# Optimization experiments

Measured on AMD Instinct MI355X. Metric: run time of the kernel, lower is better.

The kernel has to match this reference:

```python
import jax, jax.numpy as jnp
import numpy as np

H = 512; NH = 8; L = 2; NPRED = 26; MAXF = 5; FF = 4 * H


def _ln(x, w, b, eps=1e-5):
    m = x.mean(-1, keepdims=True)
    v = ((x - m) ** 2).mean(-1, keepdims=True)
    return (x - m) / jnp.sqrt(v + eps) * w + b


def _gelu(x):
    return jax.nn.gelu(x, approximate=False)


def _mha(q_in, kv_in, in_w, in_b, out_w, out_b, nh=NH):
    # PyTorch nn.MultiheadAttention math (batch_first), no mask, eval mode.
    h = q_in.shape[-1]; dh = h // nh
    Wq, Wk, Wv = in_w[:h], in_w[h:2 * h], in_w[2 * h:]
    bq, bk, bv = in_b[:h], in_b[h:2 * h], in_b[2 * h:]
    B, Tq, _ = q_in.shape
    Tk = kv_in.shape[1]
    q = (q_in @ Wq.T + bq).reshape(B, Tq, nh, dh)
    k = (kv_in @ Wk.T + bk).reshape(B, Tk, nh, dh)
    v = (kv_in @ Wv.T + bv).reshape(B, Tk, nh, dh)
    s = jnp.einsum('bqhd,bkhd->bhqk', q, k) / jnp.sqrt(jnp.asarray(dh, q.dtype))
    a = jax.nn.softmax(s, axis=-1)
    o = jnp.einsum('bhqk,bkhd->bqhd', a, v).reshape(B, Tq, h)
    return o @ out_w.T + out_b


def setup_inputs():
    key = jax.random.key(0)
    ks = iter(jax.random.split(key, 48))
    r = lambda *s: jax.random.normal(next(ks), s, jnp.float32) * 0.02
    inp = {
        'temporal_context': jax.random.normal(next(ks), (16, 10, H), jnp.float32),
        'object_features': jax.random.normal(next(ks), (16, 20, H), jnp.float32),
        'future_queries': r(MAXF, H),
        'sa_in_w': r(L, 3 * H, H), 'sa_in_b': jnp.zeros((L, 3 * H), jnp.float32),
        'sa_out_w': r(L, H, H), 'sa_out_b': jnp.zeros((L, H), jnp.float32),
        'ca_in_w': r(L, 3 * H, H), 'ca_in_b': jnp.zeros((L, 3 * H), jnp.float32),
        'ca_out_w': r(L, H, H), 'ca_out_b': jnp.zeros((L, H), jnp.float32),
        'ff1_w': r(L, FF, H), 'ff1_b': jnp.zeros((L, FF), jnp.float32),
        'ff2_w': r(L, H, FF), 'ff2_b': jnp.zeros((L, H), jnp.float32),
        'n1_w': jnp.ones((L, H), jnp.float32), 'n1_b': jnp.zeros((L, H), jnp.float32),
        'n2_w': jnp.ones((L, H), jnp.float32), 'n2_b': jnp.zeros((L, H), jnp.float32),
        'n3_w': jnp.ones((L, H), jnp.float32), 'n3_b': jnp.zeros((L, H), jnp.float32),
        'norm_w': jnp.ones((H,), jnp.float32), 'norm_b': jnp.zeros((H,), jnp.float32),
        'pe1_w': r(H, 3 * H), 'pe1_b': jnp.zeros((H,), jnp.float32),
        'pe2_w': r(H, H), 'pe2_b': jnp.zeros((H,), jnp.float32),
        'pred_w': r(NPRED, H), 'pred_b': jnp.zeros((NPRED,), jnp.float32),
        'ex_w': r(1, H), 'ex_b': jnp.zeros((1,), jnp.float32),
        'num_future_frames': 5,
    }
    return inp


def reference(temporal_context, object_features, future_queries, sa_in_w, sa_in_b,
              sa_out_w, sa_out_b, ca_in_w, ca_in_b, ca_out_w, ca_out_b,
              ff1_w, ff1_b, ff2_w, ff2_b, n1_w, n1_b, n2_w, n2_b, n3_w, n3_b,
              norm_w, norm_b, pe1_w, pe1_b, pe2_w, pe2_b, pred_w, pred_b,
              ex_w, ex_b, num_future_frames):
    B = temporal_context.shape[0]
    Fh = num_future_frames
    # Future queries expanded over batch -> TransformerDecoder (post-norm, gelu, eval)
    x = jnp.broadcast_to(future_queries[:Fh][None], (B, Fh, H))
    mem = temporal_context
    for l in range(L):
        x = _ln(x + _mha(x, x, sa_in_w[l], sa_in_b[l], sa_out_w[l], sa_out_b[l]), n1_w[l], n1_b[l])
        x = _ln(x + _mha(x, mem, ca_in_w[l], ca_in_b[l], ca_out_w[l], ca_out_b[l]), n2_w[l], n2_b[l])
        ff = _gelu(x @ ff1_w[l].T + ff1_b[l]) @ ff2_w[l].T + ff2_b[l]
        x = _ln(x + ff, n3_w[l], n3_b[l])
    ctx = _ln(x, norm_w, norm_b)  # (B, F, H)
    # Vectorized (i, j) pair construction, i != j, in the original loop order
    N = object_features.shape[1]
    ii, jj = np.nonzero(~np.eye(N, dtype=bool))  # row-major == for i: for j: skip i==j
    P = ii.shape[0]
    subj = object_features[:, ii]  # (B, P, H)
    obj = object_features[:, jj]   # (B, P, H)
    pair = jnp.concatenate([
        jnp.broadcast_to(subj[:, None], (B, Fh, P, H)),
        jnp.broadcast_to(obj[:, None], (B, Fh, P, H)),
        jnp.broadcast_to(ctx[:, :, None], (B, Fh, P, H)),
    ], axis=-1)  # (B, F, P, 3H)
    enc = _gelu(pair @ pe1_w.T + pe1_b) @ pe2_w.T + pe2_b  # (B, F, P, H)
    predicate_logits = enc @ pred_w.T + pred_b  # (B, F, P, 26)
    existence_logits = enc @ ex_w.T + ex_b      # (B, F, P, 1)
    return predicate_logits, existence_logits
```

## Files before the change

kernel.cpp:

```cpp
#include <hip/hip_runtime.h>
#include <math.h>

#define HD 512
#define FFD 2048
#define FH 5
#define TM 10
#define NO 20
#define NP 380
#define PRED_N 790400

#define XM_PLAIN 0
#define XM_GELU  1
#define XM_FQ    2
#define XM_LN    3
#define XM_LN2   4

typedef short bf16x8 __attribute__((ext_vector_type(8)));
typedef float floatx4 __attribute__((ext_vector_type(4)));

__device__ __forceinline__ float gelu_f(float v) {
    return 0.5f * v * (1.0f + erff(v * 0.70710678118654752440f));
}
__device__ __forceinline__ unsigned short f2bf(float x) {
    unsigned int u = __float_as_uint(x);
    u = (u + 0x7FFFu + ((u >> 16) & 1u)) >> 16;
    return (unsigned short)u;
}

template <int XMODE>
__device__ __forceinline__ void gemm_body(
    int bx, int by, int bz,
    const float* __restrict__ X, int ldx,
    const float* __restrict__ parts, int np, int pzstr,
    const float* __restrict__ bo,
    const float* __restrict__ lw, const float* __restrict__ lb,
    const float* __restrict__ fw, const float* __restrict__ fb,
    float* __restrict__ xout, int xmod, int gps,
    const float* __restrict__ W, int ldw,
    float* __restrict__ Y, int ldy, int zyoff,
    int Klen, float* lds)
{
    float* Wt = lds;
    float* Xs = lds + 8256;
    const int RT = (XMODE >= XM_LN) ? 8 : 16;
    int t = threadIdx.x;
    int nb = bx * 128;
    int r0 = by * RT;
    int kbase = bz * Klen;
    float* Yb = Y + (size_t)bz * zyoff;
    int c = t & 31, rg = t >> 5, scs = t >> 4, q = t & 15;

    if (XMODE >= XM_LN) {
        int rl = t >> 5;
        int r  = r0 + rl;
        int c0 = (t & 31) * 16;
        int rr = xmod ? (r % xmod) : r;
        float v[16];
        #pragma unroll
        for (int u = 0; u < 16; u += 4) {
            float4 a = *(const float4*)(X + (size_t)rr * ldx + c0 + u);
            float4 bb = *(const float4*)(bo + c0 + u);
            float vx = a.x + bb.x, vy = a.y + bb.y, vz = a.z + bb.z, vw = a.w + bb.w;
            for (int zz = 0; zz < np; ++zz) {
                float4 p = *(const float4*)(parts + (size_t)zz * pzstr + (size_t)r * HD + c0 + u);
                vx += p.x; vy += p.y; vz += p.z; vw += p.w;
            }
            v[u] = vx; v[u + 1] = vy; v[u + 2] = vz; v[u + 3] = vw;
        }
        float s1 = 0, s2 = 0;
        #pragma unroll
        for (int u = 0; u < 16; ++u) { s1 += v[u]; s2 += v[u] * v[u]; }
        #pragma unroll
        for (int o = 16; o > 0; o >>= 1) {
            s1 += __shfl_down(s1, o, 32);
            s2 += __shfl_down(s2, o, 32);
        }
        s1 = __shfl(s1, 0, 32); s2 = __shfl(s2, 0, 32);
        float mean = s1 * (1.0f / HD);
        float rstd = rsqrtf(s2 * (1.0f / HD) - mean * mean + 1e-5f);
        #pragma unroll
        for (int u = 0; u < 16; ++u)
            v[u] = (v[u] - mean) * rstd * lw[c0 + u] + lb[c0 + u];
        if (xout && bz == 0 && bx == 0) {
            #pragma unroll
            for (int u = 0; u < 16; u += 4)
                *(float4*)(xout + (size_t)r * HD + c0 + u) =
                    make_float4(v[u], v[u + 1], v[u + 2], v[u + 3]);
        }
        if (XMODE == XM_LN2) {
            float t1 = 0, t2 = 0;
            #pragma unroll
            for (int u = 0; u < 16; ++u) { t1 += v[u]; t2 += v[u] * v[u]; }
            #pragma unroll
            for (int o = 16; o > 0; o >>= 1) {
                t1 += __shfl_down(t1, o, 32);
                t2 += __shfl_down(t2, o, 32);
            }
            t1 = __shfl(t1, 0, 32); t2 = __shfl(t2, 0, 32);
            float m2 = t1 * (1.0f / HD);
            float rs2 = rsqrtf(t2 * (1.0f / HD) - m2 * m2 + 1e-5f);
            #pragma unroll
            for (int u = 0; u < 16; ++u)
                v[u] = (v[u] - m2) * rs2 * fw[c0 + u] + fb[c0 + u];
        }
        #pragma unroll
        for (int u = 0; u < 16; u += 4)
            *(float4*)(Xs + rl * HD + c0 + u) =
                make_float4(v[u], v[u + 1], v[u + 2], v[u + 3]);
        __syncthreads();
    }

    float a00 = 0, a01 = 0, a02 = 0, a03 = 0;
    float a10 = 0, a11 = 0, a12 = 0, a13 = 0;

    int nch = Klen >> 6;
    float4 wreg[8];
    float4 xra, xrb, xrc;
    {
        int kg = kbase;
        #pragma unroll
        for (int p = 0; p < 8; ++p)
            wreg[p] = *(const float4*)(W + (size_t)(nb + scs + p * 16) * ldw + kg + q * 4);
        if (XMODE == XM_PLAIN) {
            xra = *(const float4*)(X + (size_t)(r0 + scs) * ldx + kg + q * 4);
        } else if (XMODE == XM_FQ) {
            xra = *(const float4*)(X + (size_t)((r0 + scs) % FH) * ldx + kg + q * 4);
        } else if (XMODE == XM_GELU) {
            const float* p0 = X + (size_t)(r0 + scs) * ldx + kg + q * 4;
            xra = *(const float4*)p0;
            xrb = *(const float4*)(p0 + gps);
            xrc = *(const float4*)(bo + kg + q * 4);
        }
    }

    for (int ch = 0; ch < nch; ++ch) {
        if (ch) __syncthreads();
        if (XMODE <= XM_FQ) {
            float4 xv;
            if (XMODE == XM_GELU) {
                xv.x = gelu_f(xra.x + xrb.x + xrc.x);
                xv.y = gelu_f(xra.y + xrb.y + xrc.y);
                xv.z = gelu_f(xra.z + xrb.z + xrc.z);
                xv.w = gelu_f(xra.w + xrb.w + xrc.w);
            } else {
                xv = xra;
            }
            *(float4*)&Xs[scs * 64 + q * 4] = xv;
        }
        #pragma unroll
        for (int p = 0; p < 8; ++p) {
            int cc = scs + p * 16;
            Wt[(q * 4 + 0) * 129 + cc] = wreg[p].x;
            Wt[(q * 4 + 1) * 129 + cc] = wreg[p].y;
            Wt[(q * 4 + 2) * 129 + cc] = wreg[p].z;
            Wt[(q * 4 + 3) * 129 + cc] = wreg[p].w;
        }
        __syncthreads();
        if (ch + 1 < nch) {
            int kg = kbase + (ch + 1) * 64;
            #pragma unroll
            for (int p = 0; p < 8; ++p)
                wreg[p] = *(const float4*)(W + (size_t)(nb + scs + p * 16) * ldw + kg + q * 4);
            if (XMODE == XM_PLAIN) {
                xra = *(const float4*)(X + (size_t)(r0 + scs) * ldx + kg + q * 4);
            } else if (XMODE == XM_FQ) {
                xra = *(const float4*)(X + (size_t)((r0 + scs) % FH) * ldx + kg + q * 4);
            } else if (XMODE == XM_GELU) {
                const float* p0 = X + (size_t)(r0 + scs) * ldx + kg + q * 4;
                xra = *(const float4*)p0;
                xrb = *(const float4*)(p0 + gps);
                xrc = *(const float4*)(bo + kg + q * 4);
            }
        }
        if (RT == 16) {
            const float* xr0 = &Xs[(rg * 2 + 0) * 64];
            const float* xr1 = &Xs[(rg * 2 + 1) * 64];
            #pragma unroll
            for (int k4 = 0; k4 < 16; ++k4) {
                float4 x0 = *(const float4*)(xr0 + k4 * 4);
                float4 x1 = *(const float4*)(xr1 + k4 * 4);
                const float* x0p = (const float*)&x0;
                const float* x1p = (const float*)&x1;
                #pragma unroll
                for (int i = 0; i < 4; ++i) {
                    const float* wrow = &Wt[(k4 * 4 + i) * 129 + c];
                    float w0 = wrow[0], w1 = wrow[32], w2 = wrow[64], w3 = wrow[96];
                    float xi0 = x0p[i], xi1 = x1p[i];
                    a00 = fmaf(xi0, w0, a00); a01 = fmaf(xi0, w1, a01);
                    a02 = fmaf(xi0, w2, a02); a03 = fmaf(xi0, w3, a03);
                    a10 = fmaf(xi1, w0, a10); a11 = fmaf(xi1, w1, a11);
                    a12 = fmaf(xi1, w2, a12); a13 = fmaf(xi1, w3, a13);
                }
            }
        } else {
            const float* xr0 = &Xs[rg * HD + kbase + ch * 64];
            #pragma unroll
            for (int k4 = 0; k4 < 16; ++k4) {
                float4 x0 = *(const float4*)(xr0 + k4 * 4);
                const float* x0p = (const float*)&x0;
                #pragma unroll
                for (int i = 0; i < 4; ++i) {
                    const float* wrow = &Wt[(k4 * 4 + i) * 129 + c];
                    float xi0 = x0p[i];
                    a00 = fmaf(xi0, wrow[0],  a00);
                    a01 = fmaf(xi0, wrow[32], a01);
                    a02 = fmaf(xi0, wrow[64], a02);
                    a03 = fmaf(xi0, wrow[96], a03);
                }
            }
        }
    }
    if (RT == 16) {
        float* yr = Yb + (size_t)(r0 + rg * 2) * ldy + nb + c;
        yr[0] = a00; yr[32] = a01; yr[64] = a02; yr[96] = a03;
        yr += ldy;
        yr[0] = a10; yr[32] = a11; yr[64] = a12; yr[96] = a13;
    } else {
        float* yr = Yb + (size_t)(r0 + rg) * ldy + nb + c;
        yr[0] = a00; yr[32] = a01; yr[64] = a02; yr[96] = a03;
    }
}

template <int XMODE>
__global__ __launch_bounds__(256) void k_gemm(
    const float* __restrict__ X, int ldx,
    const float* __restrict__ parts, int np, int pzstr,
    const float* __restrict__ bo,
    const float* __restrict__ lw, const float* __restrict__ lb,
    const float* __restrict__ fw, const float* __restrict__ fb,
    float* __restrict__ xout, int xmod, int gps,
    const float* __restrict__ W, int ldw,
    float* __restrict__ Y, int ldy, int zyoff, int Klen)
{
    __shared__ float lds[(XMODE >= XM_LN) ? 12352 : 9280];
    gemm_body<XMODE>(blockIdx.x, blockIdx.y, blockIdx.z, X, ldx, parts, np, pzstr,
                     bo, lw, lb, fw, fb, xout, xmod, gps, W, ldw, Y, ldy, zyoff,
                     Klen, lds);
}

__device__ void mprep(int m, const float* __restrict__ pe2_w, const float* __restrict__ pe2_b,
                      const float* __restrict__ pred_w, const float* __restrict__ pred_b,
                      const float* __restrict__ ex_w, const float* __restrict__ ex_b,
                      unsigned short* __restrict__ Mbf, float* __restrict__ cb, float* lds)
{
    int t = threadIdx.x;
    if (m < 16) {
        int dl = t & 31, ec = t >> 5;
        int d = m * 32 + dl;
        float acc[27];
        #pragma unroll
        for (int k = 0; k < 27; ++k) acc[k] = 0.f;
        for (int e = ec * 64; e < ec * 64 + 64; ++e) {
            float wv = pe2_w[(size_t)e * HD + d];
            #pragma unroll
            for (int k = 0; k < 26; ++k) acc[k] = fmaf(wv, pred_w[k * HD + e], acc[k]);
            acc[26] = fmaf(wv, ex_w[e], acc[26]);
        }
        #pragma unroll
        for (int k = 0; k < 27; ++k) lds[(ec * 32 + dl) * 27 + k] = acc[k];
        __syncthreads();
        for (int idx = t; idx < 1024; idx += 256) {
            int dl2 = idx >> 5, k = idx & 31;
            float s = 0.f;
            if (k < 27) {
                #pragma unroll
                for (int e = 0; e < 8; ++e) s += lds[(e * 32 + dl2) * 27 + k];
            }
            int quad = dl2 >> 3, j = dl2 & 7;
            int nt = k >> 4, n15 = k & 15;
            int lane = quad * 16 + n15;
            Mbf[((size_t)(m * 2 + nt) * 64 + lane) * 8 + j] = f2bf(s);
        }
    } else {
        int g = t >> 3, li = t & 7;
        if (g < 27) {
            const float* wo = (g < 26) ? (pred_w + g * HD) : ex_w;
            float a = 0.f;
            for (int e = li; e < HD; e += 8) a += pe2_b[e] * wo[e];
            a += __shfl_down(a, 4, 8);
            a += __shfl_down(a, 2, 8);
            a += __shfl_down(a, 1, 8);
            if (li == 0) cb[g] = a + ((g < 26) ? pred_b[g] : ex_b[0]);
        }
    }
}

__global__ __launch_bounds__(256) void k_prep(
    const float* __restrict__ objf, const float* __restrict__ temporal,
    const float* __restrict__ pe1_w, const float* __restrict__ ca_in_w,
    const float* __restrict__ pe2_w, const float* __restrict__ pe2_b,
    const float* __restrict__ pred_w, const float* __restrict__ pred_b,
    const float* __restrict__ ex_w, const float* __restrict__ ex_b,
    float* __restrict__ SOp, float* __restrict__ kvb,
    unsigned short* __restrict__ Mbf, float* __restrict__ cb)
{
    __shared__ float lds[9280];
    int blk = blockIdx.x;
    if (blk < 320) {
        int zw = blk & 1, zk = (blk >> 1) & 1, ct = (blk >> 2) & 3, y = blk >> 4;
        gemm_body<XM_PLAIN>(ct, y, zk, objf, HD, nullptr, 0, 0,
                            nullptr, nullptr, nullptr, nullptr, nullptr,
                            nullptr, 0, 0,
                            pe1_w + zw * 512, 1536,
                            SOp + zw * 512, 1024, 327680, 256, lds);
    } else if (blk < 640) {
        int s = blk - 320;
        int ct = s & 7, l = (s >> 3) & 1, zk = (s >> 4) & 1, y = s >> 5;
        gemm_body<XM_PLAIN>(ct, y, zk, temporal, HD, nullptr, 0, 0,
                            nullptr, nullptr, nullptr, nullptr, nullptr,
                            nullptr, 0, 0,
                            ca_in_w + (size_t)(l * 1536 + 512) * HD, HD,
                            kvb + (size_t)((zk * 2 + l) * 160) * 1024, 1024, 0, 256, lds);
    } else {
        mprep(blk - 640, pe2_w, pe2_b, pred_w, pred_b, ex_w, ex_b, Mbf, cb, lds);
    }
}

__global__ __launch_bounds__(256) void k_attnsa_proj(
    int l, const float* __restrict__ qkvp, const float* __restrict__ in_b,
    const float* __restrict__ Wout, float* __restrict__ yp)
{
    __shared__ float lds[8896];
    int bi = blockIdx.x;
    int b = bi >> 4, ct = (bi >> 2) & 3, zk = bi & 3;
    int t = threadIdx.x;
    float* qkv = lds;
    float* sc  = lds + 1920;
    float* aw  = lds + 1984;
    float* ao  = lds + 8256;
    float* Wt  = lds;
    int col0 = zk * 128;
    int c = t & 31, rg = t >> 5, scs = t >> 4, q = t & 15;
    int nb = ct * 128;

    float4 wreg[8];
    #pragma unroll
    for (int p = 0; p < 8; ++p)
        wreg[p] = *(const float4*)(Wout + (size_t)(nb + scs + p * 16) * HD + col0 + q * 4);

    for (int idx = t; idx < 480; idx += 256) {
        int m = idx / 160, r = idx - m * 160;
        int tok = r >> 5, c4 = (r & 31) * 4;
        int col = m * HD + col0 + c4;
        size_t o = (size_t)(b * FH + tok) * 1536 + col;
        float4 v = *(const float4*)(in_b + l * 1536 + col);
        #pragma unroll
        for (int z = 0; z < 4; ++z) {
            float4 p = *(const float4*)(qkvp + (size_t)z * 122880 + o);
            v.x += p.x; v.y += p.y; v.z += p.z; v.w += p.w;
        }
        *(float4*)(qkv + (m * FH + tok) * 128 + c4) = v;
    }
    __syncthreads();
    if (t < 50) {
        int hh = t / 25, r = t - hh * 25, tq = r / 5, tu = r % 5;
        float s = 0;
        for (int d = 0; d < 64; ++d)
            s += qkv[tq * 128 + hh * 64 + d] * qkv[(FH + tu) * 128 + hh * 64 + d];
        sc[t] = s * 0.125f;
    }
    __syncthreads();
    if (t < 10) {
        int base = (t / 5) * 25 + (t % 5) * 5;
        float mx = -1e30f;
        for (int u = 0; u < 5; ++u) mx = fmaxf(mx, sc[base + u]);
        float e[5], sm = 0;
        for (int u = 0; u < 5; ++u) { e[u] = expf(sc[base + u] - mx); sm += e[u]; }
        for (int u = 0; u < 5; ++u) aw[base + u] = e[u] / sm;
    }
    __syncthreads();
    for (int idx = t; idx < 640; idx += 256) {
        int tok = idx >> 7, cc = idx & 127, hh = cc >> 6;
        float s = 0;
        #pragma unroll
        for (int u = 0; u < 5; ++u)
            s += aw[hh * 25 + tok * 5 + u] * qkv[(2 * FH + u) * 128 + cc];
        ao[tok * 128 + cc] = s;
    }
    __syncthreads();

    float a0 = 0, a1 = 0, a2 = 0, a3 = 0;
    for (int ch = 0; ch < 2; ++ch) {
        if (ch) __syncthreads();
        #pragma unroll
        for (int p = 0; p < 8; ++p) {
            int cc = scs + p * 16;
            Wt[(q * 4 + 0) * 129 + cc] = wreg[p].x;
            Wt[(q * 4 + 1) * 129 + cc] = wreg[p].y;
            Wt[(q * 4 + 2) * 129 + cc] = wreg[p].z;
            Wt[(q * 4 + 3) * 129 + cc] = wreg[p].w;
        }
        __syncthreads();
        if (ch == 0) {
            #pragma unroll
            for (int p = 0; p < 8; ++p)
                wreg[p] = *(const float4*)(Wout + (size_t)(nb + scs + p * 16) * HD + col0 + 64 + q * 4);
        }
        if (rg < FH) {
            const float* xr = ao + rg * 128 + ch * 64;
            #pragma unroll
            for (int k4 = 0; k4 < 16; ++k4) {
                float4 xv = *(const float4*)(xr + k4 * 4);
                #pragma unroll
                for (int i = 0; i < 4; ++i) {
                    const float* wr = &Wt[(k4 * 4 + i) * 129 + c];
                    float x = ((const float*)&xv)[i];
                    a0 = fmaf(x, wr[0],  a0); a1 = fmaf(x, wr[32], a1);
                    a2 = fmaf(x, wr[64], a2); a3 = fmaf(x, wr[96], a3);
                }
            }
        }
    }
    if (rg < FH) {
        float* yr = yp + (size_t)zk * 40960 + (size_t)(b * FH + rg) * HD + nb + c;
        yr[0] = a0; yr[32] = a1; yr[64] = a2; yr[96] = a3;
    }
}

__global__ __launch_bounds__(256) void k_attnca_proj(
    int l, const float* __restrict__ qp, const float* __restrict__ kvb,
    const float* __restrict__ in_b, const float* __restrict__ Wout,
    float* __restrict__ yp)
{
    __shared__ float lds[8896];
    int bi = blockIdx.x;
    int b = bi >> 4, ct = (bi >> 2) & 3, zk = bi & 3;
    int t = threadIdx.x;
    float* qs = lds;
    float* kl = lds + 640;
    float* vl = lds + 1920;
    float* sc = lds + 3200;
    float* aw = lds + 3328;
    float* ao = lds + 8256;
    float* Wt = lds;
    const float* bb = in_b + l * 1536;
    int col0 = zk * 128;
    int c = t & 31, rg = t >> 5, scs = t >> 4, q = t & 15;
    int nb = ct * 128;

    float4 wreg[8];
    #pragma unroll
    for (int p = 0; p < 8; ++p)
        wreg[p] = *(const float4*)(Wout + (size_t)(nb + scs + p * 16) * HD + col0 + q * 4);

    if (t < 160) {
        int tok = t >> 5, c4 = (t & 31) * 4;
        size_t o = (size_t)(b * FH + tok) * HD + col0 + c4;
        float4 v = *(const float4*)(bb + col0 + c4);
        #pragma unroll
        for (int z = 0; z < 4; ++z) {
            float4 p = *(const float4*)(qp + (size_t)z * 40960 + o);
            v.x += p.x; v.y += p.y; v.z += p.z; v.w += p.w;
        }
        *(float4*)(qs + tok * 128 + c4) = v;
    }
    for (int idx = t; idx < 320; idx += 256) {
        int u = idx >> 5, c4 = (idx & 31) * 4;
        size_t base = (size_t)(l * 160 + b * TM + u) * 1024;
        float4 k0 = *(const float4*)(kvb + base + col0 + c4);
        float4 k1 = *(const float4*)(kvb + 327680 + base + col0 + c4);
        float4 bk = *(const float4*)(bb + 512 + col0 + c4);
        *(float4*)(kl + u * 128 + c4) =
            make_float4(k0.x + k1.x + bk.x, k0.y + k1.y + bk.y,
                        k0.z + k1.z + bk.z, k0.w + k1.w + bk.w);
        float4 v0 = *(const float4*)(kvb + base + 512 + col0 + c4);
        float4 v1 = *(const float4*)(kvb + 327680 + base + 512 + col0 + c4);
        float4 bv = *(const float4*)(bb + 1024 + col0 + c4);
        *(float4*)(vl + u * 128 + c4) =
            make_float4(v0.x + v1.x + bv.x, v0.y + v1.y + bv.y,
                        v0.z + v1.z + bv.z, v0.w + v1.w + bv.w);
    }
    __syncthreads();
    if (t < 100) {
        int hh = t / 50, r = t - hh * 50, tq = r / 10, tu = r % 10;
        float s = 0;
        for (int d = 0; d < 64; ++d)
            s += qs[tq * 128 + hh * 64 + d] * kl[tu * 128 + hh * 64 + d];
        sc[t] = s * 0.125f;
    }
    __syncthreads();
    if (t < 10) {
        int base = (t / 5) * 50 + (t % 5) * 10;
        float mx = -1e30f;
        for (int u = 0; u < TM; ++u) mx = fmaxf(mx, sc[base + u]);
        float e[TM], sm = 0;
        for (int u = 0; u < TM; ++u) { e[u] = expf(sc[base + u] - mx); sm += e[u]; }
        for (int u = 0; u < TM; ++u) aw[base + u] = e[u] / sm;
    }
    __syncthreads();
    for (int idx = t; idx < 640; idx += 256) {
        int tok = idx >> 7, cc = idx & 127, hh = cc >> 6;
        float s = 0;
        #pragma unroll
        for (int u = 0; u < TM; ++u)
            s += aw[hh * 50 + tok * 10 + u] * vl[u * 128 + cc];
        ao[tok * 128 + cc] = s;
    }
    __syncthreads();

    float a0 = 0, a1 = 0, a2 = 0, a3 = 0;
    for (int ch = 0; ch < 2; ++ch) {
        if (ch) __syncthreads();
        #pragma unroll
        for (int p = 0; p < 8; ++p) {
            int cc = scs + p * 16;
            Wt[(q * 4 + 0) * 129 + cc] = wreg[p].x;
            Wt[(q * 4 + 1) * 129 + cc] = wreg[p].y;
            Wt[(q * 4 + 2) * 129 + cc] = wreg[p].z;
            Wt[(q * 4 + 3) * 129 + cc] = wreg[p].w;
        }
        __syncthreads();
        if (ch == 0) {
            #pragma unroll
            for (int p = 0; p < 8; ++p)
                wreg[p] = *(const float4*)(Wout + (size_t)(nb + scs + p * 16) * HD + col0 + 64 + q * 4);
        }
        if (rg < FH) {
            const float* xr = ao + rg * 128 + ch * 64;
            #pragma unroll
            for (int k4 = 0; k4 < 16; ++k4) {
                float4 xv = *(const float4*)(xr + k4 * 4);
                #pragma unroll
                for (int i = 0; i < 4; ++i) {
                    const float* wr = &Wt[(k4 * 4 + i) * 129 + c];
                    float x = ((const float*)&xv)[i];
                    a0 = fmaf(x, wr[0],  a0); a1 = fmaf(x, wr[32], a1);
                    a2 = fmaf(x, wr[64], a2); a3 = fmaf(x, wr[96], a3);
                }
            }
        }
    }
    if (rg < FH) {
        float* yr = yp + (size_t)zk * 40960 + (size_t)(b * FH + rg) * HD + nb + c;
        yr[0] = a0; yr[32] = a1; yr[64] = a2; yr[96] = a3;
    }
}

__global__ __launch_bounds__(256) void k_pair(
    const float* __restrict__ SOp, const float* __restrict__ cpb,
    const float* __restrict__ pe1_b,
    const unsigned short* __restrict__ Mbf, const float* __restrict__ cb,
    float* __restrict__ out)
{
    __shared__ float lds[14964];
    int blk = blockIdx.x;
    int third = blk % 3, bf = blk / 3;
    int b = bf / FH, f = bf % FH;
    int t = threadIdx.x;
    int wv = t >> 6, lane = t & 63;
    int quad = lane >> 4, n15 = lane & 15;
    int i0 = (third == 0) ? 0 : (third == 1 ? 6 : 13);

    for (int idx = t; idx < 29 * 128; idx += 256) {
        int row = idx >> 7, c4 = (idx & 127) << 2;
        float4 v;
        if (row < 8) {
            int i = i0 + row; if (i > 19) i = 19;
            size_t o = (size_t)(b * NO + i) * 1024 + c4;
            float4 p0 = *(const float4*)(SOp + o);
            float4 p1 = *(const float4*)(SOp + 327680 + o);
            v = make_float4(p0.x + p1.x, p0.y + p1.y, p0.z + p1.z, p0.w + p1.w);
        } else if (row < 28) {
            int j = row - 8;
            size_t o = (size_t)(b * NO + j) * 1024 + 512 + c4;
            float4 p0 = *(const float4*)(SOp + o);
            float4 p1 = *(const float4*)(SOp + 327680 + o);
            v = make_float4(p0.x + p1.x, p0.y + p1.y, p0.z + p1.z, p0.w + p1.w);
        } else {
            size_t o = (size_t)(b * FH + f) * HD + c4;
            float4 s = *(const float4*)(cpb + o);
            #pragma unroll
            for (int z = 1; z < 4; ++z) {
                float4 p = *(const float4*)(cpb + (size_t)z * 40960 + o);
                s.x += p.x; s.y += p.y; s.z += p.z; s.w += p.w;
            }
            float4 pb = *(const float4*)(pe1_b + c4);
            v = make_float4(s.x + pb.x, s.y + pb.y, s.z + pb.z, s.w + pb.w);
        }
        *(float4*)(lds + row * 516 + c4) = v;
    }
    __syncthreads();

    floatx4 acc00 = {0,0,0,0}, acc01 = {0,0,0,0}, acc10 = {0,0,0,0}, acc11 = {0,0,0,0};
    for (int ks = 0; ks < 16; ++ks) {
        bf16x8 b0 = *(const bf16x8*)(Mbf + ((size_t)(ks * 2 + 0) * 64 + lane) * 8);
        bf16x8 b1 = *(const bf16x8*)(Mbf + ((size_t)(ks * 2 + 1) * 64 + lane) * 8);
        #pragma unroll
        for (int mt = 0; mt < 2; ++mt) {
            int p = third * 128 + wv * 32 + mt * 16 + n15;
            bf16x8 afr = {0, 0, 0, 0, 0, 0, 0, 0};
            if (p < NP) {
                int i = p / 19, j0 = p % 19;
                int j = j0 + (j0 >= i ? 1 : 0);
                int dof = ks * 32 + quad * 8;
                const float* Sr = lds + (i - i0) * 516 + dof;
                const float* Or = lds + (8 + j) * 516 + dof;
                const float* Cr = lds + 28 * 516 + dof;
                float4 sa = *(const float4*)Sr, sb = *(const float4*)(Sr + 4);
                float4 oa = *(const float4*)Or, ob = *(const float4*)(Or + 4);
                float4 ca = *(const float4*)Cr, cc = *(const float4*)(Cr + 4);
                union { unsigned short u[8]; bf16x8 v8; } pk;
                pk.u[0] = f2bf(gelu_f(sa.x + oa.x + ca.x));
                pk.u[1] = f2bf(gelu_f(sa.y + oa.y + ca.y));
                pk.u[2] = f2bf(gelu_f(sa.z + oa.z + ca.z));
                pk.u[3] = f2bf(gelu_f(sa.w + oa.w + ca.w));
                pk.u[4] = f2bf(gelu_f(sb.x + ob.x + cc.x));
                pk.u[5] = f2bf(gelu_f(sb.y + ob.y + cc.y));
                pk.u[6] = f2bf(gelu_f(sb.z + ob.z + cc.z));
                pk.u[7] = f2bf(gelu_f(sb.w + ob.w + cc.w));
                afr = pk.v8;
            }
            if (mt == 0) {
                acc00 = __builtin_amdgcn_mfma_f32_16x16x32_bf16(afr, b0, acc00, 0, 0, 0);
                acc01 = __builtin_amdgcn_mfma_f32_16x16x32_bf16(afr, b1, acc01, 0, 0, 0);
            } else {
                acc10 = __builtin_amdgcn_mfma_f32_16x16x32_bf16(afr, b0, acc10, 0, 0, 0);
                acc11 = __builtin_amdgcn_mfma_f32_16x16x32_bf16(afr, b1, acc11, 0, 0, 0);
            }
        }
    }
    int pbase = (b * FH + f) * NP;
    #pragma unroll
    for (int mt = 0; mt < 2; ++mt) {
        #pragma unroll
        for (int nt = 0; nt < 2; ++nt) {
            floatx4 a = (mt == 0) ? (nt == 0 ? acc00 : acc01)
                                  : (nt == 0 ? acc10 : acc11);
            int n = nt * 16 + n15;
            #pragma unroll
            for (int reg = 0; reg < 4; ++reg) {
                int p = third * 128 + wv * 32 + mt * 16 + quad * 4 + reg;
                if (p < NP && n < 27) {
                    float vout = a[reg] + cb[n];
                    if (n < 26) out[(size_t)(pbase + p) * 26 + n] = vout;
                    else        out[PRED_N + pbase + p] = vout;
                }
            }
        }
    }
}

extern "C" void kernel_launch(void* const* d_in, const int* in_sizes, int n_in,
                              void* d_out, int out_size, void* d_ws, size_t ws_size,
                              hipStream_t stream) {
    const float* temporal = (const float*)d_in[0];
    const float* objf     = (const float*)d_in[1];
    const float* fq       = (const float*)d_in[2];
    const float* sa_in_w  = (const float*)d_in[3];
    const float* sa_in_b  = (const float*)d_in[4];
    const float* sa_out_w = (const float*)d_in[5];
    const float* sa_out_b = (const float*)d_in[6];
    const float* ca_in_w  = (const float*)d_in[7];
    const float* ca_in_b  = (const float*)d_in[8];
    const float* ca_out_w = (const float*)d_in[9];
    const float* ca_out_b = (const float*)d_in[10];
    const float* ff1_w    = (const float*)d_in[11];
    const float* ff1_b    = (const float*)d_in[12];
    const float* ff2_w    = (const float*)d_in[13];
    const float* ff2_b    = (const float*)d_in[14];
    const float* n1_w     = (const float*)d_in[15];
    const float* n1_b     = (const float*)d_in[16];
    const float* n2_w     = (const float*)d_in[17];
    const float* n2_b     = (const float*)d_in[18];
    const float* n3_w     = (const float*)d_in[19];
    const float* n3_b     = (const float*)d_in[20];
    const float* norm_w   = (const float*)d_in[21];
    const float* norm_b   = (const float*)d_in[22];
    const float* pe1_w    = (const float*)d_in[23];
    const float* pe1_b    = (const float*)d_in[24];
    const float* pe2_w    = (const float*)d_in[25];
    const float* pe2_b    = (const float*)d_in[26];
    const float* pred_w   = (const float*)d_in[27];
    const float* pred_b   = (const float*)d_in[28];
    const float* ex_w     = (const float*)d_in[29];
    const float* ex_b     = (const float*)d_in[30];

    float* ws   = (float*)d_ws;
    float* x1   = ws;
    float* x2   = ws + 40960;
    float* x3   = ws + 81920;
    float* qkvp = ws + 122880;
    float* qp   = ws + 614400;
    float* yp   = ws + 778240;
    float* ffp  = ws + 1105920;
    float* kvb  = ws + 1433600;
    float* SOp  = ws + 2088960;
    float* cpb  = ws + 2744320;
    unsigned short* Mbf = (unsigned short*)(ws + 2908160);
    float* cb   = ws + 2916352;
    float* out  = (float*)d_out;

    k_prep<<<657, 256, 0, stream>>>(objf, temporal, pe1_w, ca_in_w,
                                    pe2_w, pe2_b, pred_w, pred_b, ex_w, ex_b,
                                    SOp, kvb, Mbf, cb);
    for (int l = 0; l < 2; ++l) {
        if (l == 0) {
            k_gemm<XM_FQ><<<dim3(12, 5, 4), 256, 0, stream>>>(
                fq, HD, nullptr, 0, 0, nullptr, nullptr, nullptr,
                nullptr, nullptr, nullptr, 0, 0,
                sa_in_w, HD, qkvp, 1536, 122880, 128);
        } else {
            k_gemm<XM_LN><<<dim3(12, 10, 4), 256, 0, stream>>>(
                x2, HD, yp, 8, 40960, ff2_b, n3_w, n3_b,
                nullptr, nullptr, x3, 0, 0,
                sa_in_w + 786432, HD, qkvp, 1536, 122880, 128);
        }
        k_attnsa_proj<<<256, 256, 0, stream>>>(l, qkvp, sa_in_b,
                                               sa_out_w + (size_t)l * 262144, yp);
        k_gemm<XM_LN><<<dim3(4, 10, 4), 256, 0, stream>>>(
            (l == 0 ? fq : x3), HD, yp, 4, 40960,
            sa_out_b + l * HD, n1_w + l * HD, n1_b + l * HD,
            nullptr, nullptr, x1, (l == 0 ? FH : 0), 0,
            ca_in_w + (size_t)l * 786432, HD, qp, HD, 40960, 128);
        k_attnca_proj<<<256, 256, 0, stream>>>(l, qp, kvb, ca_in_b,
                                               ca_out_w + (size_t)l * 262144, yp);
        k_gemm<XM_LN><<<dim3(16, 10, 2), 256, 0, stream>>>(
            x1, HD, yp, 4, 40960,
            ca_out_b + l * HD, n2_w + l * HD, n2_b + l * HD,
            nullptr, nullptr, x2, 0, 0,
            ff1_w + (size_t)l * 1048576, HD, ffp, FFD, 163840, 256);
        k_gemm<XM_GELU><<<dim3(4, 5, 8), 256, 0, stream>>>(
            ffp, FFD, nullptr, 0, 0, ff1_b + l * FFD,
            nullptr, nullptr, nullptr, nullptr, nullptr, 0, 163840,
            ff2_w + (size_t)l * 1048576, FFD, yp, HD, 40960, 256);
    }
    k_gemm<XM_LN2><<<dim3(4, 10, 4), 256, 0, stream>>>(
        x2, HD, yp, 8, 40960, ff2_b + HD, n3_w + HD, n3_b + HD,
        norm_w, norm_b, nullptr, 0, 0,
        pe1_w + 1024, 1536, cpb, HD, 40960, 128);
    k_pair<<<240, 256, 0, stream>>>(SOp, cpb, pe1_b, Mbf, cb, out);
}
```

Measured before the change: 381.0 us.

## Fold first QKV GEMM into prep, deepen split-K, stage mprep weights in LDS

The layer-0 self-attention QKV projection, which depends only on future_queries, now runs inside k_prep as extra blocks, so one launch disappears. The mprep blocks move to the front of the grid, and their inner product stages pred_w/ex_w through LDS with float4 reads. Several GEMMs double their split-K factor (halving K per split) to spread work over more blocks, and the consumers now sum 8 or 16 partials instead of 4 or 8. The workspace is compacted so qkvp, qp and ffp share one buffer. The cost is more partial-sum traffic and longer reduction loops in the consumers.

```diff
diff --git a/kernel.cpp b/kernel.cpp
--- a/kernel.cpp
+++ b/kernel.cpp
@@ -250,12 +250,33 @@
         float acc[27];
         #pragma unroll
         for (int k = 0; k < 27; ++k) acc[k] = 0.f;
-        for (int e = ec * 64; e < ec * 64 + 64; ++e) {
-            float wv = pe2_w[(size_t)e * HD + d];
-            #pragma unroll
-            for (int k = 0; k < 26; ++k) acc[k] = fmaf(wv, pred_w[k * HD + e], acc[k]);
-            acc[26] = fmaf(wv, ex_w[e], acc[26]);
-        }
+        for (int sub = 0; sub < 2; ++sub) {
+            __syncthreads();
+            for (int idx = t; idx < 1728; idx += 256) {
+                int g = idx / 216, r = idx - g * 216;
+                int k = r >> 3, f4 = (r & 7) * 4;
+                int eoff = g * 64 + sub * 32 + f4;
+                float4 pv = (k < 26) ? *(const float4*)(pred_w + k * HD + eoff)
+                                     : *(const float4*)(ex_w + eoff);
+                *(float4*)(lds + g * 864 + k * 32 + f4) = pv;
+            }
+            __syncthreads();
+            int ebase = ec * 64 + sub * 32;
+            const float* ps = lds + ec * 864;
+            #pragma unroll 2
+            for (int e4 = 0; e4 < 8; ++e4) {
+                float w0 = pe2_w[(size_t)(ebase + e4 * 4 + 0) * HD + d];
+                float w1 = pe2_w[(size_t)(ebase + e4 * 4 + 1) * HD + d];
+                float w2 = pe2_w[(size_t)(ebase + e4 * 4 + 2) * HD + d];
+                float w3 = pe2_w[(size_t)(ebase + e4 * 4 + 3) * HD + d];
+                #pragma unroll
+                for (int k = 0; k < 27; ++k) {
+                    float4 pv = *(const float4*)(ps + k * 32 + e4 * 4);
+                    acc[k] += w0 * pv.x + w1 * pv.y + w2 * pv.z + w3 * pv.w;
+                }
+            }
+        }
+        __syncthreads();
         #pragma unroll
         for (int k = 0; k < 27; ++k) lds[(ec * 32 + dl) * 27 + k] = acc[k];
         __syncthreads();
@@ -287,24 +308,30 @@
 
 __global__ __launch_bounds__(256) void k_prep(
     const float* __restrict__ objf, const float* __restrict__ temporal,
+    const float* __restrict__ fq,
     const float* __restrict__ pe1_w, const float* __restrict__ ca_in_w,
+    const float* __restrict__ sa_in_w,
     const float* __restrict__ pe2_w, const float* __restrict__ pe2_b,
     const float* __restrict__ pred_w, const float* __restrict__ pred_b,
     const float* __restrict__ ex_w, const float* __restrict__ ex_b,
     float* __restrict__ SOp, float* __restrict__ kvb,
+    float* __restrict__ qkvp,
     unsigned short* __restrict__ Mbf, float* __restrict__ cb)
 {
     __shared__ float lds[9280];
     int blk = blockIdx.x;
-    if (blk < 320) {
-        int zw = blk & 1, zk = (blk >> 1) & 1, ct = (blk >> 2) & 3, y = blk >> 4;
+    if (blk < 17) {
+        mprep(blk, pe2_w, pe2_b, pred_w, pred_b, ex_w, ex_b, Mbf, cb, lds);
+    } else if (blk < 337) {
+        int s = blk - 17;
+        int zw = s & 1, zk = (s >> 1) & 1, ct = (s >> 2) & 3, y = s >> 4;
         gemm_body<XM_PLAIN>(ct, y, zk, objf, HD, nullptr, 0, 0,
                             nullptr, nullptr, nullptr, nullptr, nullptr,
                             nullptr, 0, 0,
                             pe1_w + zw * 512, 1536,
                             SOp + zw * 512, 1024, 327680, 256, lds);
-    } else if (blk < 640) {
-        int s = blk - 320;
+    } else if (blk < 657) {
+        int s = blk - 337;
         int ct = s & 7, l = (s >> 3) & 1, zk = (s >> 4) & 1, y = s >> 5;
         gemm_body<XM_PLAIN>(ct, y, zk, temporal, HD, nullptr, 0, 0,
                             nullptr, nullptr, nullptr, nullptr, nullptr,
@@ -312,7 +339,12 @@
                             ca_in_w + (size_t)(l * 1536 + 512) * HD, HD,
                             kvb + (size_t)((zk * 2 + l) * 160) * 1024, 1024, 0, 256, lds);
     } else {
-        mprep(blk - 640, pe2_w, pe2_b, pred_w, pred_b, ex_w, ex_b, Mbf, cb, lds);
+        int s = blk - 657;
+        int x = s % 12, y = (s / 12) % 5, z = s / 60;
+        gemm_body<XM_FQ>(x, y, z, fq, HD, nullptr, 0, 0,
+                         nullptr, nullptr, nullptr, nullptr, nullptr,
+                         nullptr, 0, 0,
+                         sa_in_w, HD, qkvp, 1536, 122880, 128, lds);
     }
 }
 
@@ -448,7 +480,7 @@
         size_t o = (size_t)(b * FH + tok) * HD + col0 + c4;
         float4 v = *(const float4*)(bb + col0 + c4);
         #pragma unroll
-        for (int z = 0; z < 4; ++z) {
+        for (int z = 0; z < 8; ++z) {
             float4 p = *(const float4*)(qp + (size_t)z * 40960 + o);
             v.x += p.x; v.y += p.y; v.z += p.z; v.w += p.w;
         }
@@ -570,7 +602,7 @@
             size_t o = (size_t)(b * FH + f) * HD + c4;
             float4 s = *(const float4*)(cpb + o);
             #pragma unroll
-            for (int z = 1; z < 4; ++z) {
+            for (int z = 1; z < 8; ++z) {
                 float4 p = *(const float4*)(cpb + (size_t)z * 40960 + o);
                 s.x += p.x; s.y += p.y; s.z += p.z; s.w += p.w;
             }
@@ -679,39 +711,35 @@
     float* x1   = ws;
     float* x2   = ws + 40960;
     float* x3   = ws + 81920;
-    float* qkvp = ws + 122880;
-    float* qp   = ws + 614400;
-    float* yp   = ws + 778240;
-    float* ffp  = ws + 1105920;
-    float* kvb  = ws + 1433600;
-    float* SOp  = ws + 2088960;
-    float* cpb  = ws + 2744320;
+    float* big  = ws + 122880;
+    float* yp   = ws + 614400;
+    float* kvb  = ws + 1269760;
+    float* SOp  = ws + 1925120;
+    float* cpb  = ws + 2580480;
     unsigned short* Mbf = (unsigned short*)(ws + 2908160);
     float* cb   = ws + 2916352;
     float* out  = (float*)d_out;
-
-    k_prep<<<657, 256, 0, stream>>>(objf, temporal, pe1_w, ca_in_w,
+    float* qkvp = big;
+    float* qp   = big;
+    float* ffp  = big;
+
+    k_prep<<<897, 256, 0, stream>>>(objf, temporal, fq, pe1_w, ca_in_w, sa_in_w,
                                     pe2_w, pe2_b, pred_w, pred_b, ex_w, ex_b,
-                                    SOp, kvb, Mbf, cb);
+                                    SOp, kvb, qkvp, Mbf, cb);
     for (int l = 0; l < 2; ++l) {
-        if (l == 0) {
-            k_gemm<XM_FQ><<<dim3(12, 5, 4), 256, 0, stream>>>(
-                fq, HD, nullptr, 0, 0, nullptr, nullptr, nullptr,
-                nullptr, nullptr, nullptr, 0, 0,
-                sa_in_w, HD, qkvp, 1536, 122880, 128);
-        } else {
+        if (l == 1) {
             k_gemm<XM_LN><<<dim3(12, 10, 4), 256, 0, stream>>>(
-                x2, HD, yp, 8, 40960, ff2_b, n3_w, n3_b,
+                x2, HD, yp, 16, 40960, ff2_b, n3_w, n3_b,
                 nullptr, nullptr, x3, 0, 0,
                 sa_in_w + 786432, HD, qkvp, 1536, 122880, 128);
         }
         k_attnsa_proj<<<256, 256, 0, stream>>>(l, qkvp, sa_in_b,
                                                sa_out_w + (size_t)l * 262144, yp);
-        k_gemm<XM_LN><<<dim3(4, 10, 4), 256, 0, stream>>>(
+        k_gemm<XM_LN><<<dim3(4, 10, 8), 256, 0, stream>>>(
             (l == 0 ? fq : x3), HD, yp, 4, 40960,
             sa_out_b + l * HD, n1_w + l * HD, n1_b + l * HD,
             nullptr, nullptr, x1, (l == 0 ? FH : 0), 0,
-            ca_in_w + (size_t)l * 786432, HD, qp, HD, 40960, 128);
+            ca_in_w + (size_t)l * 786432, HD, qp, HD, 40960, 64);
         k_attnca_proj<<<256, 256, 0, stream>>>(l, qp, kvb, ca_in_b,
                                                ca_out_w + (size_t)l * 262144, yp);
         k_gemm<XM_LN><<<dim3(16, 10, 2), 256, 0, stream>>>(
@@ -719,14 +747,14 @@
             ca_out_b + l * HD, n2_w + l * HD, n2_b + l * HD,
             nullptr, nullptr, x2, 0, 0,
             ff1_w + (size_t)l * 1048576, HD, ffp, FFD, 163840, 256);
-        k_gemm<XM_GELU><<<dim3(4, 5, 8), 256, 0, stream>>>(
+        k_gemm<XM_GELU><<<dim3(4, 5, 16), 256, 0, stream>>>(
             ffp, FFD, nullptr, 0, 0, ff1_b + l * FFD,
             nullptr, nullptr, nullptr, nullptr, nullptr, 0, 163840,
-            ff2_w + (size_t)l * 1048576, FFD, yp, HD, 40960, 256);
-    }
-    k_gemm<XM_LN2><<<dim3(4, 10, 4), 256, 0, stream>>>(
-        x2, HD, yp, 8, 40960, ff2_b + HD, n3_w + HD, n3_b + HD,
+            ff2_w + (size_t)l * 1048576, FFD, yp, HD, 40960, 128);
+    }
+    k_gemm<XM_LN2><<<dim3(4, 10, 8), 256, 0, stream>>>(
+        x2, HD, yp, 16, 40960, ff2_b + HD, n3_w + HD, n3_b + HD,
         norm_w, norm_b, nullptr, 0, 0,
-        pe1_w + 1024, 1536, cpb, HD, 40960, 128);
+        pe1_w + 1024, 1536, cpb, HD, 40960, 64);
     k_pair<<<240, 256, 0, stream>>>(SOp, cpb, pe1_b, Mbf, cb, out);
 }
```

New measurement: 368.3 us. 1.03x faster.
